# Kernel tuning notes

Hardware: AMD Instinct MI355X
Metric: run time of the kernel (lower is better)

The kernel has to match this reference:

```python
import jax, jax.numpy as jnp
import numpy as np

# static config (matches init_kwargs / input_specs)
B, S, D, H, DH = 4, 2048, 2048, 16, 128
MAX_LEN = 1024  # round_up_to_multiple_of_256(max ragged length); lengths below max at 1024
ROPE_BASE = 10000.0


def setup_inputs() -> dict:
    key = jax.random.key(0)
    ks = jax.random.split(key, 8)
    q_src = jax.random.normal(ks[0], (B, MAX_LEN, D), jnp.float32)
    k_src = jax.random.normal(ks[1], (B, S, D), jnp.float32)
    v_src = jax.random.normal(ks[2], (B, S, D), jnp.float32)
    std = 1.0 / np.sqrt(D)
    Wq = jax.random.normal(ks[3], (D, H * DH), jnp.float32) * std
    Wk = jax.random.normal(ks[4], (D, H * DH), jnp.float32) * std
    Wv = jax.random.normal(ks[5], (D, H * DH), jnp.float32) * std
    Wo = jax.random.normal(ks[6], (H * DH, D), jnp.float32) * (1.0 / np.sqrt(H * DH))
    # mask[0]: causal bool [B,S,S]; mask[1]: full position ids [B,S]
    mask0 = jnp.broadcast_to(jnp.tril(jnp.ones((S, S), bool)), (B, S, S))
    pos_full = jnp.broadcast_to(jnp.arange(S, dtype=jnp.int32), (B, S))
    # ragged skip_mask: row i keeps lengths[i] random positions (max 1024 -> MAX_LEN)
    lengths = jnp.array([1024, 896, 768, 640], jnp.int32)
    scores = jax.random.uniform(ks[7], (B, S))
    ranks = jnp.argsort(jnp.argsort(scores, axis=1), axis=1)
    skip_mask = ranks < lengths[:, None]
    return {"q_src": q_src, "k_src": k_src, "v_src": v_src,
            "Wq": Wq, "Wk": Wk, "Wv": Wv, "Wo": Wo,
            "mask0": mask0, "pos_full": pos_full, "skip_mask": skip_mask}


def _rope(x, positions):
    # x: [B,H,L,DH], positions: [B,L] int -> rotary embedding on full head dim
    dh = x.shape[-1]
    inv_freq = 1.0 / (ROPE_BASE ** (jnp.arange(0, dh, 2, dtype=jnp.float32) / dh))
    freqs = positions.astype(jnp.float32)[:, :, None] * inv_freq      # [B,L,dh/2]
    emb = jnp.concatenate([freqs, freqs], axis=-1)[:, None]           # [B,1,L,dh]
    x1, x2 = jnp.split(x, 2, axis=-1)
    rot = jnp.concatenate([-x2, x1], axis=-1)                         # rotate_half
    return x * jnp.cos(emb) + rot * jnp.sin(emb)


def reference(q_src, k_src, v_src, Wq, Wk, Wv, Wo, mask0, pos_full, skip_mask):
    def heads(x, W):
        y = x @ W
        return y.reshape(x.shape[0], x.shape[1], H, DH).transpose(0, 2, 1, 3)

    q = heads(q_src, Wq)   # [B,H,MAX_LEN,DH]
    k = heads(k_src, Wk)   # [B,H,S,DH]
    v = heads(v_src, Wv)   # [B,H,S,DH]

    # _trim_attention_mask: gather kept rows (True-first, stable order), pad to MAX_LEN
    order = jnp.argsort(jnp.where(skip_mask, 0, 1), axis=1)[:, :MAX_LEN]  # [B,MAX_LEN]
    n = skip_mask.sum(axis=1)                                             # ragged lengths
    valid = jnp.arange(MAX_LEN)[None, :] < n[:, None]                     # [B,MAX_LEN]
    amask = jnp.take_along_axis(mask0, order[:, :, None], axis=1) & valid[:, :, None]
    pos_trim = jnp.where(valid, jnp.take_along_axis(pos_full, order, axis=1), 0)

    # RoPE: trimmed positions for q, full positions for k
    q = _rope(q, pos_trim)
    k = _rope(k, pos_full)

    # masked SDPA; fully-masked (padded) query rows -> zero output
    logits = jnp.einsum('bhld,bhsd->bhls', q, k) / np.sqrt(DH).astype(np.float32)
    logits = jnp.where(amask[:, None], logits, jnp.finfo(logits.dtype).min)
    probs = jax.nn.softmax(logits, axis=-1) * valid[:, None, :, None]
    ctx = jnp.einsum('bhls,bhsd->bhld', probs, v)                         # [B,H,MAX_LEN,DH]

    out = ctx.transpose(0, 2, 1, 3).reshape(B, MAX_LEN, H * DH) @ Wo     # [B,MAX_LEN,D]
    return out
```

## Files before the change

kernel.cpp:

```cpp
#include <hip/hip_runtime.h>

#define BB 4
#define SS 2048
#define DD 2048
#define HH 16
#define DHD 128
#define MAXL 1024

typedef __bf16 bf16x8 __attribute__((ext_vector_type(8)));
typedef float f32x4 __attribute__((ext_vector_type(4)));
typedef unsigned int u32_as1 __attribute__((address_space(1)));
typedef unsigned int u32_as3 __attribute__((address_space(3)));

__device__ __forceinline__ unsigned short f2bf(float f) {
  unsigned int u = __builtin_bit_cast(unsigned int, f);
  u += 0x7fffu + ((u >> 16) & 1u);
  return (unsigned short)(u >> 16);
}
__device__ __forceinline__ float bf2f(unsigned short h) {
  unsigned int u = ((unsigned int)h) << 16;
  return __builtin_bit_cast(float, u);
}
union U4 { uint4 u; bf16x8 b; };
__device__ __forceinline__ bf16x8 ldfrag(const unsigned short* p) {
  U4 x; x.u = *(const uint4*)p; return x.b;
}
__device__ __forceinline__ void gl_lds16(const void* g, void* l) {
  __builtin_amdgcn_global_load_lds((const u32_as1*)g, (u32_as3*)l, 16, 0, 0);
}

template <int C>
__device__ __forceinline__ float dppf(float x) {
  return __builtin_bit_cast(float,
      __builtin_amdgcn_mov_dpp(__builtin_bit_cast(int, x), C, 0xF, 0xF, true));
}
__device__ __forceinline__ float rmax16(float x) {
  x = fmaxf(x, dppf<0xB1>(x));
  x = fmaxf(x, dppf<0x4E>(x));
  x = fmaxf(x, dppf<0x141>(x));
  x = fmaxf(x, dppf<0x140>(x));
  return x;
}
__device__ __forceinline__ float radd16(float x) {
  x += dppf<0xB1>(x);
  x += dppf<0x4E>(x);
  x += dppf<0x141>(x);
  x += dppf<0x140>(x);
  return x;
}

__global__ void build_pos(const int* __restrict__ skip, int* __restrict__ posk,
                          int* __restrict__ nval) {
  int b = blockIdx.x, t = threadIdx.x;
  __shared__ int cnts[64], offs[64];
  const int* row = skip + b * SS;
  int c = 0;
  for (int i = 0; i < 32; i++) c += (row[t * 32 + i] != 0);
  cnts[t] = c;
  __syncthreads();
  if (t == 0) {
    int run = 0;
    for (int i = 0; i < 64; i++) { offs[i] = run; run += cnts[i]; }
    nval[b] = run > MAXL ? MAXL : run;
  }
  __syncthreads();
  int o = offs[t];
  for (int i = 0; i < 32; i++)
    if (row[t * 32 + i]) { if (o < MAXL) posk[b * MAXL + o] = t * 32 + i; o++; }
  int nb = nval[b];
  for (int l = nb + t; l < MAXL; l += 64) posk[b * MAXL + l] = -1;
}

__global__ __launch_bounds__(256) void cvt3(const float* __restrict__ q,
                                            const float* __restrict__ k,
                                            const float* __restrict__ v,
                                            unsigned short* __restrict__ oq,
                                            unsigned short* __restrict__ ok,
                                            unsigned short* __restrict__ ov) {
  const int nq = BB * MAXL * DD / 4, nk = BB * SS * DD / 4;
  int idx = blockIdx.x * 256 + threadIdx.x;
  const float* src; unsigned short* dst; int off;
  if (idx < nq) { src = q; dst = oq; off = idx; }
  else if (idx < nq + nk) { src = k; dst = ok; off = idx - nq; }
  else { src = v; dst = ov; off = idx - nq - nk; }
  float4 vv = ((const float4*)src)[off];
  ushort4 h;
  h.x = f2bf(vv.x); h.y = f2bf(vv.y); h.z = f2bf(vv.z); h.w = f2bf(vv.w);
  ((ushort4*)dst)[off] = h;
}

__global__ __launch_bounds__(256) void transpose_w4(const float* __restrict__ w0,
    const float* __restrict__ w1, const float* __restrict__ w2, const float* __restrict__ w3,
    unsigned short* __restrict__ o0, unsigned short* __restrict__ o1,
    unsigned short* __restrict__ o2, unsigned short* __restrict__ o3) {
  __shared__ __align__(16) unsigned short tile[64 * 76];
  const float* W; unsigned short* Wt;
  switch (blockIdx.z) {
    case 0: W = w0; Wt = o0; break;
    case 1: W = w1; Wt = o1; break;
    case 2: W = w2; Wt = o2; break;
    default: W = w3; Wt = o3; break;
  }
  int tx = threadIdx.x;
  int K0 = blockIdx.y * 64, N0 = blockIdx.x * 64;
  #pragma unroll
  for (int i = 0; i < 4; i++) {
    int r = (tx >> 4) + i * 16, c4 = (tx & 15) * 4;
    float4 v = *(const float4*)&W[(size_t)(K0 + r) * DD + N0 + c4];
    ushort4 h;
    h.x = f2bf(v.x); h.y = f2bf(v.y); h.z = f2bf(v.z); h.w = f2bf(v.w);
    *(ushort4*)&tile[r * 76 + c4] = h;
  }
  __syncthreads();
  #pragma unroll
  for (int i = 0; i < 4; i++) {
    int n = (tx >> 4) + i * 16, k4 = (tx & 15) * 4;
    ushort4 h;
    h.x = tile[(k4 + 0) * 76 + n];
    h.y = tile[(k4 + 1) * 76 + n];
    h.z = tile[(k4 + 2) * 76 + n];
    h.w = tile[(k4 + 3) * 76 + n];
    *(ushort4*)&Wt[(size_t)(N0 + n) * DD + K0 + k4] = h;
  }
}

template <int BM>
__global__ __launch_bounds__(512, 2) void gemm8(const unsigned short* __restrict__ A,
                                                const unsigned short* __restrict__ Bt,
                                                void* __restrict__ Cp,
                                                int M, int N, int K, int mode, int Lbits) {
  constexpr int AW = BM * 64;
  __shared__ __align__(16) unsigned short lds[(BM + 256) * 64 * 2];
  unsigned short* const Abuf = lds;
  unsigned short* const Bbuf = lds + 2 * AW;

  const int tid = threadIdx.x;
  const int lane = tid & 63, quad = lane >> 4, c = lane & 15;
  const int w = tid >> 6;
  const int wm = (w >> 2) * (BM / 2), wn = (w & 3) * 64;

  const int nwg = gridDim.x * gridDim.y;
  const int bid0 = blockIdx.y * gridDim.x + blockIdx.x;
  const int cpx = nwg >> 3;
  const int bid = (bid0 & 7) * cpx + (bid0 >> 3);
  const int bx = bid % gridDim.x;
  const int by = bid / gridDim.x;
  const size_t tm = (size_t)by * BM, tn = (size_t)bx * 256;

  constexpr int MR = BM / 32;
  f32x4 acc[MR][4] = {};

  const int trow = tid >> 3;
  const int tch = ((tid & 7) ^ (trow & 7)) * 8;
  const unsigned short* gA = A + (tm + trow) * (size_t)K + tch;
  const unsigned short* gB = Bt + (tn + trow) * (size_t)K + tch;
  constexpr int ALD = BM / 64;
  constexpr int NLD = ALD + 4;

  auto STAGE = [&](int sel, int kk) {
    unsigned short* ad = Abuf + sel * AW;
    unsigned short* bd = Bbuf + sel * 16384;
    #pragma unroll
    for (int i = 0; i < ALD; i++)
      gl_lds16(gA + kk + (size_t)(i * 64) * K, ad + i * 4096 + tid * 8);
    #pragma unroll
    for (int i = 0; i < 4; i++)
      gl_lds16(gB + kk + (size_t)(i * 64) * K, bd + i * 4096 + tid * 8);
  };

  const int nkt = K >> 6;
  STAGE(0, 0);

  for (int t = 0; t < nkt; ++t) {
    const int sel = t & 1;
    const unsigned short* as = Abuf + sel * AW;
    const unsigned short* bs = Bbuf + sel * 16384;
    if (t + 1 < nkt) {
      STAGE(sel ^ 1, (t + 1) << 6);
      asm volatile("s_waitcnt vmcnt(%0)" ::"i"(NLD) : "memory");
    } else {
      asm volatile("s_waitcnt vmcnt(0)" ::: "memory");
    }
    __builtin_amdgcn_s_barrier();

    bf16x8 a0[4][2], b01[2][2], b23[2][2];
    #pragma unroll
    for (int i = 0; i < 4; i++)
      #pragma unroll
      for (int ks = 0; ks < 2; ks++)
        a0[i][ks] = ldfrag(&as[(wm + i * 16 + c) * 64 + (((ks * 4 + quad) ^ (c & 7)) << 3)]);
    #pragma unroll
    for (int j = 0; j < 2; j++)
      #pragma unroll
      for (int ks = 0; ks < 2; ks++)
        b01[j][ks] = ldfrag(&bs[(wn + j * 16 + c) * 64 + (((ks * 4 + quad) ^ (c & 7)) << 3)]);
    __builtin_amdgcn_s_barrier();
    __builtin_amdgcn_s_setprio(1);
    #pragma unroll
    for (int i = 0; i < 4; i++)
      #pragma unroll
      for (int j = 0; j < 2; j++)
        #pragma unroll
        for (int ks = 0; ks < 2; ks++)
          acc[i][j] = __builtin_amdgcn_mfma_f32_16x16x32_bf16(a0[i][ks], b01[j][ks], acc[i][j], 0, 0, 0);
    __builtin_amdgcn_s_setprio(0);
    __builtin_amdgcn_s_barrier();
    #pragma unroll
    for (int j = 0; j < 2; j++)
      #pragma unroll
      for (int ks = 0; ks < 2; ks++)
        b23[j][ks] = ldfrag(&bs[(wn + 32 + j * 16 + c) * 64 + (((ks * 4 + quad) ^ (c & 7)) << 3)]);
    __builtin_amdgcn_s_barrier();
    __builtin_amdgcn_s_setprio(1);
    #pragma unroll
    for (int i = 0; i < 4; i++)
      #pragma unroll
      for (int j = 0; j < 2; j++)
        #pragma unroll
        for (int ks = 0; ks < 2; ks++)
          acc[i][2 + j] = __builtin_amdgcn_mfma_f32_16x16x32_bf16(a0[i][ks], b23[j][ks], acc[i][2 + j], 0, 0, 0);
    __builtin_amdgcn_s_setprio(0);
    __builtin_amdgcn_s_barrier();

    if constexpr (BM == 256) {
      bf16x8 a1[4][2];
      #pragma unroll
      for (int i = 0; i < 4; i++)
        #pragma unroll
        for (int ks = 0; ks < 2; ks++)
          a1[i][ks] = ldfrag(&as[(wm + 64 + i * 16 + c) * 64 + (((ks * 4 + quad) ^ (c & 7)) << 3)]);
      __builtin_amdgcn_s_barrier();
      __builtin_amdgcn_s_setprio(1);
      #pragma unroll
      for (int i = 0; i < 4; i++)
        #pragma unroll
        for (int j = 0; j < 2; j++)
          #pragma unroll
          for (int ks = 0; ks < 2; ks++)
            acc[4 + i][j] = __builtin_amdgcn_mfma_f32_16x16x32_bf16(a1[i][ks], b01[j][ks], acc[4 + i][j], 0, 0, 0);
      __builtin_amdgcn_s_setprio(0);
      __builtin_amdgcn_s_barrier();
      __builtin_amdgcn_s_setprio(1);
      #pragma unroll
      for (int i = 0; i < 4; i++)
        #pragma unroll
        for (int j = 0; j < 2; j++)
          #pragma unroll
          for (int ks = 0; ks < 2; ks++)
            acc[4 + i][2 + j] = __builtin_amdgcn_mfma_f32_16x16x32_bf16(a1[i][ks], b23[j][ks], acc[4 + i][2 + j], 0, 0, 0);
      __builtin_amdgcn_s_setprio(0);
      __builtin_amdgcn_s_barrier();
    }
  }

  if (mode == 1) {
    float* Cf = (float*)Cp;
    #pragma unroll
    for (int i = 0; i < MR; i++)
      #pragma unroll
      for (int j = 0; j < 4; j++)
        #pragma unroll
        for (int r = 0; r < 4; r++) {
          size_t m = tm + wm + i * 16 + quad * 4 + r;
          size_t n = tn + wn + j * 16 + c;
          Cf[m * N + n] = acc[i][j][r];
        }
    return;
  }
  unsigned short* Cb = (unsigned short*)Cp;
  unsigned short* ep = lds + w * 4352;
  constexpr int MH = BM / 128;
  if (mode == 0) {
    const size_t Lmask = ((size_t)1 << Lbits) - 1;
    #pragma unroll
    for (int mh = 0; mh < MH; mh++) {
      #pragma unroll
      for (int i = 0; i < 4; i++)
        #pragma unroll
        for (int j = 0; j < 4; j++)
          #pragma unroll
          for (int r = 0; r < 4; r++)
            ep[(i * 16 + quad * 4 + r) * 68 + j * 16 + c] = f2bf(acc[mh * 4 + i][j][r]);
      #pragma unroll
      for (int it = 0; it < 8; it++) {
        int chunk = it * 64 + lane;
        int ml = chunk >> 3, nc = (chunk & 7) * 8;
        uint4 val = *(const uint4*)&ep[ml * 68 + nc];
        size_t m = tm + wm + mh * 64 + ml, n = tn + wn + nc;
        size_t b = m >> Lbits, l = m & Lmask, h = n >> 7, d = n & 127;
        *(uint4*)&Cb[(((b * HH + h) << Lbits) + l) * 128 + d] = val;
      }
    }
  } else {
    #pragma unroll
    for (int mh = 0; mh < MH; mh++) {
      #pragma unroll
      for (int i = 0; i < 4; i++)
        #pragma unroll
        for (int j = 0; j < 4; j++)
          #pragma unroll
          for (int r = 0; r < 4; r++)
            ep[(j * 16 + c) * 68 + i * 16 + quad * 4 + r] = f2bf(acc[mh * 4 + i][j][r]);
      #pragma unroll
      for (int it = 0; it < 8; it++) {
        int chunk = it * 64 + lane;
        int nl = chunk >> 3, mc = (chunk & 7) * 8;
        uint4 val = *(const uint4*)&ep[nl * 68 + mc];
        size_t n = tn + wn + nl, m = tm + wm + mh * 64 + mc;
        size_t b = m >> 11, s = m & 2047, h = n >> 7, d = n & 127;
        *(uint4*)&Cb[((b * HH + h) * 128 + d) * SS + s] = val;
      }
    }
  }
}

__global__ __launch_bounds__(256) void rope2(unsigned short* __restrict__ xq,
                                             unsigned short* __restrict__ xk,
                                             const int* __restrict__ posk) {
  const int Nq = BB * HH * MAXL * 64;
  int gid = blockIdx.x * 256 + threadIdx.x;
  unsigned short* x; int Lbits, idx, use_posk;
  if (gid < Nq) { x = xq; Lbits = 10; use_posk = 1; idx = gid; }
  else { x = xk; Lbits = 11; use_posk = 0; idx = gid - Nq; }
  int d = idx & 63;
  int rest = idx >> 6;
  int l = rest & ((1 << Lbits) - 1);
  int bh = rest >> Lbits;
  int b = bh >> 4;
  int p = use_posk ? posk[(b << 10) + l] : l;
  float ang = (float)p * __expf(-(float)d * 0.14391156831212787f);
  float sn, cs;
  __sincosf(ang, &sn, &cs);
  size_t base = (size_t)rest * 128;
  float x1 = bf2f(x[base + d]), x2 = bf2f(x[base + d + 64]);
  x[base + d]      = f2bf(x1 * cs - x2 * sn);
  x[base + d + 64] = f2bf(x2 * cs + x1 * sn);
}

__global__ __launch_bounds__(256) void attn_kernel(const unsigned short* __restrict__ qp,
                                                   const unsigned short* __restrict__ kp,
                                                   const unsigned short* __restrict__ vtp,
                                                   const int* __restrict__ posk,
                                                   const int* __restrict__ nval,
                                                   unsigned short* __restrict__ ctx) {
  __shared__ __align__(16) unsigned short k_s[2][64 * 128];
  __shared__ __align__(16) unsigned short vt_s[2][128 * 64];
  __shared__ __align__(16) unsigned short p_s[4 * 16 * 72];
  __shared__ int km_s[64];

  const int tid = threadIdx.x;
  const int w = tid >> 6, lane = tid & 63, quad = lane >> 4, c = lane & 15;
  const int bh = blockIdx.x, b = bh >> 4, h = bh & 15;
  const int qbase = blockIdx.y * 64;
  const int nb = nval[b];

  if (tid < 64) {
    int l = qbase + tid;
    km_s[tid] = (l < nb) ? posk[(b << 10) + l] : -1;
  }
  __syncthreads();

  const unsigned short* qg = qp + (((size_t)bh << 10) + qbase) * 128;
  bf16x8 aq[4];
  #pragma unroll
  for (int ks = 0; ks < 4; ks++)
    aq[ks] = ldfrag(&qg[(size_t)(w * 16 + c) * 128 + ks * 32 + quad * 8]);

  int lv = nb - 1 - qbase; lv = lv > 63 ? 63 : lv;
  const int tile_kmax = (lv >= 0) ? km_s[lv] : -1;
  const int nkt = (tile_kmax >= 0) ? ((tile_kmax >> 6) + 1) : 0;

  int wl = w * 16 + 15; if (wl > lv) wl = lv;
  const int wkmax = (wl >= w * 16) ? km_s[wl] : -1;

  int km[4];
  #pragma unroll
  for (int r = 0; r < 4; r++) km[r] = km_s[w * 16 + quad * 4 + r];

  const int srow = tid >> 4;
  const int kswz = (tid & 15) ^ (srow & 7);
  const unsigned short* kgp = kp + ((size_t)bh << 11) * 128 + (size_t)srow * 128 + kswz * 8;
  const int dvrow = tid >> 3;
  const int vswz = (tid & 7) ^ (dvrow & 7);
  const unsigned short* vgp = vtp + ((size_t)bh * 128 + dvrow) * SS + vswz * 8;

  auto STG = [&](int buf, int kb) {
    #pragma unroll
    for (int i = 0; i < 4; i++)
      gl_lds16(kgp + ((size_t)kb + i * 16) * 128, &k_s[buf][(i * 256 + tid) * 8]);
    #pragma unroll
    for (int i = 0; i < 4; i++)
      gl_lds16(vgp + (size_t)kb + (size_t)i * 32 * SS, &vt_s[buf][(i * 256 + tid) * 8]);
  };

  float m_i[4], l_i[4];
  #pragma unroll
  for (int r = 0; r < 4; r++) { m_i[r] = -1e30f; l_i[r] = 0.f; }
  f32x4 o[8];
  #pragma unroll
  for (int dj = 0; dj < 8; dj++) o[dj] = (f32x4){0.f, 0.f, 0.f, 0.f};

  if (nkt > 0) STG(0, 0);

  for (int kt = 0; kt < nkt; kt++) {
    const int cur = kt & 1;
    const int kb = kt * 64;
    if (kt + 1 < nkt) {
      STG(cur ^ 1, kb + 64);
      asm volatile("s_waitcnt vmcnt(8)" ::: "memory");
    } else {
      asm volatile("s_waitcnt vmcnt(0)" ::: "memory");
    }
    __builtin_amdgcn_s_barrier();

    if (kb <= wkmax) {
      f32x4 sa[4];
      #pragma unroll
      for (int j = 0; j < 4; j++) {
        sa[j] = (f32x4){0.f, 0.f, 0.f, 0.f};
        #pragma unroll
        for (int ks = 0; ks < 4; ks++) {
          bf16x8 bk = ldfrag(&k_s[cur][((j * 16 + c) << 7) + (((ks * 4 + quad) ^ (c & 7)) << 3)]);
          sa[j] = __builtin_amdgcn_mfma_f32_16x16x32_bf16(aq[ks], bk, sa[j], 0, 0, 0);
        }
      }

      const float scale = 0.08838834764831843f;
      float mt[4] = {-1e30f, -1e30f, -1e30f, -1e30f};
      #pragma unroll
      for (int j = 0; j < 4; j++) {
        int key = kb + j * 16 + c;
        #pragma unroll
        for (int r = 0; r < 4; r++) {
          float v = (key <= km[r]) ? sa[j][r] * scale : -1e30f;
          sa[j][r] = v;
          mt[r] = fmaxf(mt[r], v);
        }
      }
      float al[4], rs[4];
      #pragma unroll
      for (int r = 0; r < 4; r++) {
        mt[r] = rmax16(mt[r]);
        float mn = fmaxf(m_i[r], mt[r]);
        al[r] = __expf(m_i[r] - mn);
        m_i[r] = mn;
        rs[r] = 0.f;
      }
      #pragma unroll
      for (int j = 0; j < 4; j++)
        #pragma unroll
        for (int r = 0; r < 4; r++) {
          float pv = __expf(sa[j][r] - m_i[r]);
          sa[j][r] = pv;
          rs[r] += pv;
        }
      #pragma unroll
      for (int r = 0; r < 4; r++) {
        rs[r] = radd16(rs[r]);
        l_i[r] = l_i[r] * al[r] + rs[r];
      }
      #pragma unroll
      for (int dj = 0; dj < 8; dj++)
        #pragma unroll
        for (int r = 0; r < 4; r++) o[dj][r] *= al[r];

      #pragma unroll
      for (int j = 0; j < 4; j++)
        #pragma unroll
        for (int r = 0; r < 4; r++)
          p_s[w * 1152 + (quad * 4 + r) * 72 + j * 16 + c] = f2bf(sa[j][r]);

      #pragma unroll
      for (int ks2 = 0; ks2 < 2; ks2++) {
        bf16x8 ap = ldfrag(&p_s[w * 1152 + c * 72 + ks2 * 32 + quad * 8]);
        #pragma unroll
        for (int dj = 0; dj < 8; dj++) {
          bf16x8 bv = ldfrag(&vt_s[cur][((dj * 16 + c) << 6) + (((ks2 * 4 + quad) ^ (c & 7)) << 3)]);
          o[dj] = __builtin_amdgcn_mfma_f32_16x16x32_bf16(ap, bv, o[dj], 0, 0, 0);
        }
      }
    }
    __builtin_amdgcn_s_barrier();
  }

  #pragma unroll
  for (int r = 0; r < 4; r++) {
    int l = qbase + w * 16 + quad * 4 + r;
    bool ok = (l < nb);
    float inv = ok ? (1.0f / l_i[r]) : 0.0f;
    #pragma unroll
    for (int dj = 0; dj < 8; dj++)
      ctx[(((size_t)b << 10) + l) * (size_t)DD + h * 128 + dj * 16 + c] =
          f2bf(ok ? o[dj][r] * inv : 0.0f);
  }
}

extern "C" void kernel_launch(void* const* d_in, const int* in_sizes, int n_in,
                              void* d_out, int out_size, void* d_ws, size_t ws_size,
                              hipStream_t stream) {
  const float* q_src = (const float*)d_in[0];
  const float* k_src = (const float*)d_in[1];
  const float* v_src = (const float*)d_in[2];
  const float* Wq = (const float*)d_in[3];
  const float* Wk = (const float*)d_in[4];
  const float* Wv = (const float*)d_in[5];
  const float* Wo = (const float*)d_in[6];
  const int* skip = (const int*)d_in[9];

  char* p = (char*)d_ws;
  auto alloc = [&](size_t bytes) -> char* {
    char* r = p;
    p += (bytes + 255) & ~(size_t)255;
    return r;
  };
  unsigned short* a_q  = (unsigned short*)alloc((size_t)BB * MAXL * DD * 2);
  unsigned short* a_k  = (unsigned short*)alloc((size_t)BB * SS * DD * 2);
  unsigned short* a_v  = (unsigned short*)alloc((size_t)BB * SS * DD * 2);
  unsigned short* wt_q = (unsigned short*)alloc((size_t)DD * DD * 2);
  unsigned short* wt_k = (unsigned short*)alloc((size_t)DD * DD * 2);
  unsigned short* wt_v = (unsigned short*)alloc((size_t)DD * DD * 2);
  unsigned short* wt_o = (unsigned short*)alloc((size_t)DD * DD * 2);
  unsigned short* q_pro = (unsigned short*)alloc((size_t)BB * HH * MAXL * DHD * 2);
  unsigned short* k_pro = (unsigned short*)alloc((size_t)BB * HH * SS * DHD * 2);
  unsigned short* v_t   = (unsigned short*)alloc((size_t)BB * HH * SS * DHD * 2);
  int* posk = (int*)alloc((size_t)BB * MAXL * 4);
  int* nval = (int*)alloc(64);
  unsigned short* ctx = a_q;

  build_pos<<<BB, 64, 0, stream>>>(skip, posk, nval);
  cvt3<<<(BB * MAXL * DD + 2 * BB * SS * DD) / (4 * 256), 256, 0, stream>>>(
      q_src, k_src, v_src, a_q, a_k, a_v);
  transpose_w4<<<dim3(32, 32, 4), 256, 0, stream>>>(Wq, Wk, Wv, Wo, wt_q, wt_k, wt_v, wt_o);

  gemm8<128><<<dim3(8, 32), 512, 0, stream>>>(a_q, wt_q, q_pro, BB * MAXL, DD, DD, 0, 10);
  gemm8<256><<<dim3(8, 32), 512, 0, stream>>>(a_k, wt_k, k_pro, BB * SS, DD, DD, 0, 11);
  gemm8<256><<<dim3(8, 32), 512, 0, stream>>>(a_v, wt_v, v_t, BB * SS, DD, DD, 2, 11);

  rope2<<<(BB * HH * (MAXL + SS) * 64) / 256, 256, 0, stream>>>(q_pro, k_pro, posk);

  attn_kernel<<<dim3(BB * HH, MAXL / 64), 256, 0, stream>>>(q_pro, k_pro, v_t, posk, nval, ctx);

  gemm8<128><<<dim3(8, 32), 512, 0, stream>>>(ctx, wt_o, d_out, BB * MAXL, DD, DD, 1, 0);
}
```

Baseline: 692.7 us.

## Fuse prep kernels, fold softmax scale into RoPE, double query rows per attention block

Merges the three prep kernels (bf16 convert, weight transpose, position build) into one launch to cut launch overhead. Folds the 1/sqrt(d)·log2(e) scale into the RoPE pass for q, so attention uses exp2 with no per-element scaling. The attention kernel now handles 128 query rows per block, with each wave keeping two 16-row groups, so every staged K/V tile is reused twice, and it skips masking on tiles that are fully visible. It also reorders one MFMA loop in the GEMM. The trade-off is higher register pressure and half as many attention blocks, which lowers occupancy and parallelism.

```diff
diff --git a/kernel.cpp b/kernel.cpp
--- a/kernel.cpp
+++ b/kernel.cpp
@@ -49,78 +49,86 @@
   return x;
 }
 
-__global__ void build_pos(const int* __restrict__ skip, int* __restrict__ posk,
-                          int* __restrict__ nval) {
-  int b = blockIdx.x, t = threadIdx.x;
+#define NCVT 40960
+#define NTW  4096
+__global__ __launch_bounds__(256) void prep(
+    const float* __restrict__ q, const float* __restrict__ k, const float* __restrict__ v,
+    unsigned short* __restrict__ oq, unsigned short* __restrict__ ok,
+    unsigned short* __restrict__ ov,
+    const float* __restrict__ w0, const float* __restrict__ w1,
+    const float* __restrict__ w2, const float* __restrict__ w3,
+    unsigned short* __restrict__ t0, unsigned short* __restrict__ t1,
+    unsigned short* __restrict__ t2, unsigned short* __restrict__ t3,
+    const int* __restrict__ skip, int* __restrict__ posk, int* __restrict__ nval) {
+  __shared__ __align__(16) unsigned short tile[64 * 76];
   __shared__ int cnts[64], offs[64];
-  const int* row = skip + b * SS;
-  int c = 0;
-  for (int i = 0; i < 32; i++) c += (row[t * 32 + i] != 0);
-  cnts[t] = c;
-  __syncthreads();
-  if (t == 0) {
-    int run = 0;
-    for (int i = 0; i < 64; i++) { offs[i] = run; run += cnts[i]; }
-    nval[b] = run > MAXL ? MAXL : run;
-  }
-  __syncthreads();
-  int o = offs[t];
-  for (int i = 0; i < 32; i++)
-    if (row[t * 32 + i]) { if (o < MAXL) posk[b * MAXL + o] = t * 32 + i; o++; }
-  int nb = nval[b];
-  for (int l = nb + t; l < MAXL; l += 64) posk[b * MAXL + l] = -1;
-}
-
-__global__ __launch_bounds__(256) void cvt3(const float* __restrict__ q,
-                                            const float* __restrict__ k,
-                                            const float* __restrict__ v,
-                                            unsigned short* __restrict__ oq,
-                                            unsigned short* __restrict__ ok,
-                                            unsigned short* __restrict__ ov) {
-  const int nq = BB * MAXL * DD / 4, nk = BB * SS * DD / 4;
-  int idx = blockIdx.x * 256 + threadIdx.x;
-  const float* src; unsigned short* dst; int off;
-  if (idx < nq) { src = q; dst = oq; off = idx; }
-  else if (idx < nq + nk) { src = k; dst = ok; off = idx - nq; }
-  else { src = v; dst = ov; off = idx - nq - nk; }
-  float4 vv = ((const float4*)src)[off];
-  ushort4 h;
-  h.x = f2bf(vv.x); h.y = f2bf(vv.y); h.z = f2bf(vv.z); h.w = f2bf(vv.w);
-  ((ushort4*)dst)[off] = h;
-}
-
-__global__ __launch_bounds__(256) void transpose_w4(const float* __restrict__ w0,
-    const float* __restrict__ w1, const float* __restrict__ w2, const float* __restrict__ w3,
-    unsigned short* __restrict__ o0, unsigned short* __restrict__ o1,
-    unsigned short* __restrict__ o2, unsigned short* __restrict__ o3) {
-  __shared__ __align__(16) unsigned short tile[64 * 76];
-  const float* W; unsigned short* Wt;
-  switch (blockIdx.z) {
-    case 0: W = w0; Wt = o0; break;
-    case 1: W = w1; Wt = o1; break;
-    case 2: W = w2; Wt = o2; break;
-    default: W = w3; Wt = o3; break;
-  }
-  int tx = threadIdx.x;
-  int K0 = blockIdx.y * 64, N0 = blockIdx.x * 64;
-  #pragma unroll
-  for (int i = 0; i < 4; i++) {
-    int r = (tx >> 4) + i * 16, c4 = (tx & 15) * 4;
-    float4 v = *(const float4*)&W[(size_t)(K0 + r) * DD + N0 + c4];
-    ushort4 h;
-    h.x = f2bf(v.x); h.y = f2bf(v.y); h.z = f2bf(v.z); h.w = f2bf(v.w);
-    *(ushort4*)&tile[r * 76 + c4] = h;
-  }
-  __syncthreads();
-  #pragma unroll
-  for (int i = 0; i < 4; i++) {
-    int n = (tx >> 4) + i * 16, k4 = (tx & 15) * 4;
-    ushort4 h;
-    h.x = tile[(k4 + 0) * 76 + n];
-    h.y = tile[(k4 + 1) * 76 + n];
-    h.z = tile[(k4 + 2) * 76 + n];
-    h.w = tile[(k4 + 3) * 76 + n];
-    *(ushort4*)&Wt[(size_t)(N0 + n) * DD + K0 + k4] = h;
+  const int bid = blockIdx.x;
+  const int tx = threadIdx.x;
+
+  if (bid < NCVT) {
+    const int nq = BB * MAXL * DD / 4, nk = BB * SS * DD / 4;
+    int idx = bid * 256 + tx;
+    const float* src; unsigned short* dst; int off;
+    if (idx < nq) { src = q; dst = oq; off = idx; }
+    else if (idx < nq + nk) { src = k; dst = ok; off = idx - nq; }
+    else { src = v; dst = ov; off = idx - nq - nk; }
+    float4 vv = ((const float4*)src)[off];
+    ushort4 hh;
+    hh.x = f2bf(vv.x); hh.y = f2bf(vv.y); hh.z = f2bf(vv.z); hh.w = f2bf(vv.w);
+    ((ushort4*)dst)[off] = hh;
+  } else if (bid < NCVT + NTW) {
+    int rem = bid - NCVT;
+    int z = rem >> 10, r2 = rem & 1023;
+    int bx = r2 & 31, by = r2 >> 5;
+    const float* W; unsigned short* Wt;
+    switch (z) {
+      case 0: W = w0; Wt = t0; break;
+      case 1: W = w1; Wt = t1; break;
+      case 2: W = w2; Wt = t2; break;
+      default: W = w3; Wt = t3; break;
+    }
+    int K0 = by * 64, N0 = bx * 64;
+    #pragma unroll
+    for (int i = 0; i < 4; i++) {
+      int r = (tx >> 4) + i * 16, c4 = (tx & 15) * 4;
+      float4 vv = *(const float4*)&W[(size_t)(K0 + r) * DD + N0 + c4];
+      ushort4 hh;
+      hh.x = f2bf(vv.x); hh.y = f2bf(vv.y); hh.z = f2bf(vv.z); hh.w = f2bf(vv.w);
+      *(ushort4*)&tile[r * 76 + c4] = hh;
+    }
+    __syncthreads();
+    #pragma unroll
+    for (int i = 0; i < 4; i++) {
+      int n = (tx >> 4) + i * 16, k4 = (tx & 15) * 4;
+      ushort4 hh;
+      hh.x = tile[(k4 + 0) * 76 + n];
+      hh.y = tile[(k4 + 1) * 76 + n];
+      hh.z = tile[(k4 + 2) * 76 + n];
+      hh.w = tile[(k4 + 3) * 76 + n];
+      *(ushort4*)&Wt[(size_t)(N0 + n) * DD + K0 + k4] = hh;
+    }
+  } else {
+    int b = bid - (NCVT + NTW);
+    const int* row = skip + b * SS;
+    if (tx < 64) {
+      int c = 0;
+      for (int i = 0; i < 32; i++) c += (row[tx * 32 + i] != 0);
+      cnts[tx] = c;
+    }
+    __syncthreads();
+    if (tx == 0) {
+      int run = 0;
+      for (int i = 0; i < 64; i++) { offs[i] = run; run += cnts[i]; }
+      nval[b] = run > MAXL ? MAXL : run;
+    }
+    __syncthreads();
+    if (tx < 64) {
+      int o = offs[tx];
+      for (int i = 0; i < 32; i++)
+        if (row[tx * 32 + i]) { if (o < MAXL) posk[b * MAXL + o] = tx * 32 + i; o++; }
+      int nb = nval[b];
+      for (int l = nb + tx; l < MAXL; l += 64) posk[b * MAXL + l] = -1;
+    }
   }
 }
 
@@ -215,9 +223,9 @@
     #pragma unroll
     for (int i = 0; i < 4; i++)
       #pragma unroll
-      for (int j = 0; j < 2; j++)
-        #pragma unroll
-        for (int ks = 0; ks < 2; ks++)
+      for (int ks = 0; ks < 2; ks++)
+        #pragma unroll
+        for (int j = 0; j < 2; j++)
           acc[i][2 + j] = __builtin_amdgcn_mfma_f32_16x16x32_bf16(a0[i][ks], b23[j][ks], acc[i][2 + j], 0, 0, 0);
     __builtin_amdgcn_s_setprio(0);
     __builtin_amdgcn_s_barrier();
@@ -317,6 +325,7 @@
 __global__ __launch_bounds__(256) void rope2(unsigned short* __restrict__ xq,
                                              unsigned short* __restrict__ xk,
                                              const int* __restrict__ posk) {
+  constexpr float QSCL = (float)(0.08838834764831843 * 1.4426950408889634);
   const int Nq = BB * HH * MAXL * 64;
   int gid = blockIdx.x * 256 + threadIdx.x;
   unsigned short* x; int Lbits, idx, use_posk;
@@ -331,10 +340,11 @@
   float ang = (float)p * __expf(-(float)d * 0.14391156831212787f);
   float sn, cs;
   __sincosf(ang, &sn, &cs);
+  float S = use_posk ? QSCL : 1.0f;
   size_t base = (size_t)rest * 128;
   float x1 = bf2f(x[base + d]), x2 = bf2f(x[base + d + 64]);
-  x[base + d]      = f2bf(x1 * cs - x2 * sn);
-  x[base + d + 64] = f2bf(x2 * cs + x1 * sn);
+  x[base + d]      = f2bf((x1 * cs - x2 * sn) * S);
+  x[base + d + 64] = f2bf((x2 * cs + x1 * sn) * S);
 }
 
 __global__ __launch_bounds__(256) void attn_kernel(const unsigned short* __restrict__ qp,
@@ -346,36 +356,44 @@
   __shared__ __align__(16) unsigned short k_s[2][64 * 128];
   __shared__ __align__(16) unsigned short vt_s[2][128 * 64];
   __shared__ __align__(16) unsigned short p_s[4 * 16 * 72];
-  __shared__ int km_s[64];
+  __shared__ int km_s[128];
 
   const int tid = threadIdx.x;
   const int w = tid >> 6, lane = tid & 63, quad = lane >> 4, c = lane & 15;
   const int bh = blockIdx.x, b = bh >> 4, h = bh & 15;
-  const int qbase = blockIdx.y * 64;
+  const int qbase = blockIdx.y << 7;
   const int nb = nval[b];
 
-  if (tid < 64) {
+  if (tid < 128) {
     int l = qbase + tid;
     km_s[tid] = (l < nb) ? posk[(b << 10) + l] : -1;
   }
   __syncthreads();
 
-  const unsigned short* qg = qp + (((size_t)bh << 10) + qbase) * 128;
-  bf16x8 aq[4];
+  int lv = nb - 1 - qbase; lv = lv > 127 ? 127 : lv;
+  const int nkt = (lv >= 0) ? ((km_s[lv] >> 6) + 1) : 0;
+
+  int wkx[2], kmn[2], km[2][4];
   #pragma unroll
-  for (int ks = 0; ks < 4; ks++)
-    aq[ks] = ldfrag(&qg[(size_t)(w * 16 + c) * 128 + ks * 32 + quad * 8]);
-
-  int lv = nb - 1 - qbase; lv = lv > 63 ? 63 : lv;
-  const int tile_kmax = (lv >= 0) ? km_s[lv] : -1;
-  const int nkt = (tile_kmax >= 0) ? ((tile_kmax >> 6) + 1) : 0;
-
-  int wl = w * 16 + 15; if (wl > lv) wl = lv;
-  const int wkmax = (wl >= w * 16) ? km_s[wl] : -1;
-
-  int km[4];
+  for (int s = 0; s < 2; s++) {
+    int bs = s * 64 + w * 16;
+    bool whas = (bs <= lv);
+    int wl = bs + 15; if (wl > lv) wl = lv;
+    wkx[s] = whas ? km_s[wl] : -1;
+    kmn[s] = whas ? km_s[bs] : -1;
+    #pragma unroll
+    for (int r = 0; r < 4; r++) km[s][r] = km_s[bs + quad * 4 + r];
+  }
+
+  const unsigned short* qg = qp + ((size_t)bh << 10) * 128;
+  bf16x8 aq[2][4];
   #pragma unroll
-  for (int r = 0; r < 4; r++) km[r] = km_s[w * 16 + quad * 4 + r];
+  for (int s = 0; s < 2; s++)
+    #pragma unroll
+    for (int ks = 0; ks < 4; ks++)
+      aq[s][ks] = ldfrag(&qg[(size_t)(qbase + s * 64 + w * 16 + c) * 128 + ks * 32 + quad * 8]);
+  asm volatile("" : "+v"(aq[0][0]), "+v"(aq[0][1]), "+v"(aq[0][2]), "+v"(aq[0][3]),
+                    "+v"(aq[1][0]), "+v"(aq[1][1]), "+v"(aq[1][2]), "+v"(aq[1][3]) :: "memory");
 
   const int srow = tid >> 4;
   const int kswz = (tid & 15) ^ (srow & 7);
@@ -393,12 +411,16 @@
       gl_lds16(vgp + (size_t)kb + (size_t)i * 32 * SS, &vt_s[buf][(i * 256 + tid) * 8]);
   };
 
-  float m_i[4], l_i[4];
+  float m_i[2][4], l_i[2][4];
   #pragma unroll
-  for (int r = 0; r < 4; r++) { m_i[r] = -1e30f; l_i[r] = 0.f; }
-  f32x4 o[8];
+  for (int s = 0; s < 2; s++)
+    #pragma unroll
+    for (int r = 0; r < 4; r++) { m_i[s][r] = -1e30f; l_i[s][r] = 0.f; }
+  f32x4 o[2][8];
   #pragma unroll
-  for (int dj = 0; dj < 8; dj++) o[dj] = (f32x4){0.f, 0.f, 0.f, 0.f};
+  for (int s = 0; s < 2; s++)
+    #pragma unroll
+    for (int dj = 0; dj < 8; dj++) o[s][dj] = (f32x4){0.f, 0.f, 0.f, 0.f};
 
   if (nkt > 0) STG(0, 0);
 
@@ -413,86 +435,97 @@
     }
     __builtin_amdgcn_s_barrier();
 
-    if (kb <= wkmax) {
-      f32x4 sa[4];
-      #pragma unroll
-      for (int j = 0; j < 4; j++) {
-        sa[j] = (f32x4){0.f, 0.f, 0.f, 0.f};
-        #pragma unroll
-        for (int ks = 0; ks < 4; ks++) {
-          bf16x8 bk = ldfrag(&k_s[cur][((j * 16 + c) << 7) + (((ks * 4 + quad) ^ (c & 7)) << 3)]);
-          sa[j] = __builtin_amdgcn_mfma_f32_16x16x32_bf16(aq[ks], bk, sa[j], 0, 0, 0);
+    #pragma unroll
+    for (int s = 0; s < 2; s++) {
+      if (kb <= wkx[s]) {
+        f32x4 sa[4];
+        #pragma unroll
+        for (int j = 0; j < 4; j++) {
+          sa[j] = (f32x4){0.f, 0.f, 0.f, 0.f};
+          #pragma unroll
+          for (int ks = 0; ks < 4; ks++) {
+            bf16x8 bk = ldfrag(&k_s[cur][((j * 16 + c) << 7) + (((ks * 4 + quad) ^ (c & 7)) << 3)]);
+            sa[j] = __builtin_amdgcn_mfma_f32_16x16x32_bf16(aq[s][ks], bk, sa[j], 0, 0, 0);
+          }
+        }
+
+        float mt[4] = {-1e30f, -1e30f, -1e30f, -1e30f};
+        if (kb + 63 <= kmn[s]) {
+          #pragma unroll
+          for (int j = 0; j < 4; j++)
+            #pragma unroll
+            for (int r = 0; r < 4; r++) mt[r] = fmaxf(mt[r], sa[j][r]);
+        } else {
+          #pragma unroll
+          for (int j = 0; j < 4; j++) {
+            int key = kb + j * 16 + c;
+            #pragma unroll
+            for (int r = 0; r < 4; r++) {
+              float v = (key <= km[s][r]) ? sa[j][r] : -1e30f;
+              sa[j][r] = v;
+              mt[r] = fmaxf(mt[r], v);
+            }
+          }
+        }
+        float al[4], rs[4];
+        #pragma unroll
+        for (int r = 0; r < 4; r++) {
+          mt[r] = rmax16(mt[r]);
+          float mn = fmaxf(m_i[s][r], mt[r]);
+          al[r] = __builtin_exp2f(m_i[s][r] - mn);
+          m_i[s][r] = mn;
+          rs[r] = 0.f;
+        }
+        #pragma unroll
+        for (int j = 0; j < 4; j++)
+          #pragma unroll
+          for (int r = 0; r < 4; r++) {
+            float pv = __builtin_exp2f(sa[j][r] - m_i[s][r]);
+            sa[j][r] = pv;
+            rs[r] += pv;
+          }
+        #pragma unroll
+        for (int r = 0; r < 4; r++) {
+          rs[r] = radd16(rs[r]);
+          l_i[s][r] = l_i[s][r] * al[r] + rs[r];
+        }
+        #pragma unroll
+        for (int dj = 0; dj < 8; dj++)
+          #pragma unroll
+          for (int r = 0; r < 4; r++) o[s][dj][r] *= al[r];
+
+        #pragma unroll
+        for (int j = 0; j < 4; j++)
+          #pragma unroll
+          for (int r = 0; r < 4; r++)
+            p_s[w * 1152 + (quad * 4 + r) * 72 + j * 16 + c] = f2bf(sa[j][r]);
+
+        #pragma unroll
+        for (int ks2 = 0; ks2 < 2; ks2++) {
+          bf16x8 ap = ldfrag(&p_s[w * 1152 + c * 72 + ks2 * 32 + quad * 8]);
+          #pragma unroll
+          for (int dj = 0; dj < 8; dj++) {
+            bf16x8 bv = ldfrag(&vt_s[cur][((dj * 16 + c) << 6) + (((ks2 * 4 + quad) ^ (c & 7)) << 3)]);
+            o[s][dj] = __builtin_amdgcn_mfma_f32_16x16x32_bf16(ap, bv, o[s][dj], 0, 0, 0);
+          }
         }
       }
-
-      const float scale = 0.08838834764831843f;
-      float mt[4] = {-1e30f, -1e30f, -1e30f, -1e30f};
-      #pragma unroll
-      for (int j = 0; j < 4; j++) {
-        int key = kb + j * 16 + c;
-        #pragma unroll
-        for (int r = 0; r < 4; r++) {
-          float v = (key <= km[r]) ? sa[j][r] * scale : -1e30f;
-          sa[j][r] = v;
-          mt[r] = fmaxf(mt[r], v);
-        }
-      }
-      float al[4], rs[4];
-      #pragma unroll
-      for (int r = 0; r < 4; r++) {
-        mt[r] = rmax16(mt[r]);
-        float mn = fmaxf(m_i[r], mt[r]);
-        al[r] = __expf(m_i[r] - mn);
-        m_i[r] = mn;
-        rs[r] = 0.f;
-      }
-      #pragma unroll
-      for (int j = 0; j < 4; j++)
-        #pragma unroll
-        for (int r = 0; r < 4; r++) {
-          float pv = __expf(sa[j][r] - m_i[r]);
-          sa[j][r] = pv;
-          rs[r] += pv;
-        }
-      #pragma unroll
-      for (int r = 0; r < 4; r++) {
-        rs[r] = radd16(rs[r]);
-        l_i[r] = l_i[r] * al[r] + rs[r];
-      }
+    }
+    __builtin_amdgcn_s_barrier();
+  }
+
+  #pragma unroll
+  for (int s = 0; s < 2; s++)
+    #pragma unroll
+    for (int r = 0; r < 4; r++) {
+      int l = qbase + s * 64 + w * 16 + quad * 4 + r;
+      bool ok = (l < nb);
+      float inv = ok ? (1.0f / l_i[s][r]) : 0.0f;
       #pragma unroll
       for (int dj = 0; dj < 8; dj++)
-        #pragma unroll
-        for (int r = 0; r < 4; r++) o[dj][r] *= al[r];
-
-      #pragma unroll
-      for (int j = 0; j < 4; j++)
-        #pragma unroll
-        for (int r = 0; r < 4; r++)
-          p_s[w * 1152 + (quad * 4 + r) * 72 + j * 16 + c] = f2bf(sa[j][r]);
-
-      #pragma unroll
-      for (int ks2 = 0; ks2 < 2; ks2++) {
-        bf16x8 ap = ldfrag(&p_s[w * 1152 + c * 72 + ks2 * 32 + quad * 8]);
-        #pragma unroll
-        for (int dj = 0; dj < 8; dj++) {
-          bf16x8 bv = ldfrag(&vt_s[cur][((dj * 16 + c) << 6) + (((ks2 * 4 + quad) ^ (c & 7)) << 3)]);
-          o[dj] = __builtin_amdgcn_mfma_f32_16x16x32_bf16(ap, bv, o[dj], 0, 0, 0);
-        }
-      }
-    }
-    __builtin_amdgcn_s_barrier();
-  }
-
-  #pragma unroll
-  for (int r = 0; r < 4; r++) {
-    int l = qbase + w * 16 + quad * 4 + r;
-    bool ok = (l < nb);
-    float inv = ok ? (1.0f / l_i[r]) : 0.0f;
-    #pragma unroll
-    for (int dj = 0; dj < 8; dj++)
-      ctx[(((size_t)b << 10) + l) * (size_t)DD + h * 128 + dj * 16 + c] =
-          f2bf(ok ? o[dj][r] * inv : 0.0f);
-  }
+        ctx[(((size_t)b << 10) + l) * (size_t)DD + h * 128 + dj * 16 + c] =
+            f2bf(ok ? o[s][dj][r] * inv : 0.0f);
+    }
 }
 
 extern "C" void kernel_launch(void* const* d_in, const int* in_sizes, int n_in,
@@ -527,10 +560,9 @@
   int* nval = (int*)alloc(64);
   unsigned short* ctx = a_q;
 
-  build_pos<<<BB, 64, 0, stream>>>(skip, posk, nval);
-  cvt3<<<(BB * MAXL * DD + 2 * BB * SS * DD) / (4 * 256), 256, 0, stream>>>(
-      q_src, k_src, v_src, a_q, a_k, a_v);
-  transpose_w4<<<dim3(32, 32, 4), 256, 0, stream>>>(Wq, Wk, Wv, Wo, wt_q, wt_k, wt_v, wt_o);
+  prep<<<NCVT + NTW + BB, 256, 0, stream>>>(q_src, k_src, v_src, a_q, a_k, a_v,
+                                            Wq, Wk, Wv, Wo, wt_q, wt_k, wt_v, wt_o,
+                                            skip, posk, nval);
 
   gemm8<128><<<dim3(8, 32), 512, 0, stream>>>(a_q, wt_q, q_pro, BB * MAXL, DD, DD, 0, 10);
   gemm8<256><<<dim3(8, 32), 512, 0, stream>>>(a_k, wt_k, k_pro, BB * SS, DD, DD, 0, 11);
@@ -538,7 +570,7 @@
 
   rope2<<<(BB * HH * (MAXL + SS) * 64) / 256, 256, 0, stream>>>(q_pro, k_pro, posk);
 
-  attn_kernel<<<dim3(BB * HH, MAXL / 64), 256, 0, stream>>>(q_pro, k_pro, v_t, posk, nval, ctx);
+  attn_kernel<<<dim3(BB * HH, MAXL / 128), 256, 0, stream>>>(q_pro, k_pro, v_t, posk, nval, ctx);
 
   gemm8<128><<<dim3(8, 32), 512, 0, stream>>>(ctx, wt_o, d_out, BB * MAXL, DD, DD, 1, 0);
 }
```

New measurement: 709.6 us. 1.02x slower.
